# Performance work log

Measured on AMD Instinct MI355X. Metric: run time of the kernel, lower is better.

Reference implementation:

```python
import jax, jax.numpy as jnp
import numpy as np

B, S, D = 2, 2048, 1024
H = 16
DH = D // H  # 64

def setup_inputs() -> dict:
    key = jax.random.key(0)
    ks = jax.random.split(key, 7)
    sc = 1.0 / np.sqrt(DH)
    return {
        "sequences": jax.random.normal(ks[0], (B, S, D), dtype=jnp.float32),
        "Wq": jax.random.normal(ks[1], (H, DH, DH), dtype=jnp.float32) * sc,
        "bq": jax.random.normal(ks[2], (H, DH), dtype=jnp.float32) * 0.02,
        "Wk": jax.random.normal(ks[3], (H, DH, DH), dtype=jnp.float32) * sc,
        "bk": jax.random.normal(ks[4], (H, DH), dtype=jnp.float32) * 0.02,
        "Wv": jax.random.normal(ks[5], (H, DH, DH), dtype=jnp.float32) * sc,
        "bv": jax.random.normal(ks[6], (H, DH), dtype=jnp.float32) * 0.02,
    }

def reference(sequences, Wq, bq, Wk, bk, Wv, bv):
    b, s, _ = sequences.shape
    x = sequences.reshape(b, s, H, DH)  # [B,S,H,Dh]
    # torch Linear: y = x @ W^T + b; W is [out,in] => einsum contracts input dim d
    q = jnp.einsum("bshd,hed->bshe", x, Wq) + bq  # [B,S,H,Dh]
    k = jnp.einsum("bshd,hed->bshe", x, Wk) + bk
    v = jnp.einsum("bshd,hed->bshe", x, Wv) + bv
    scores = jnp.einsum("bshd,bthd->bhst", q, k) / jnp.sqrt(jnp.float32(DH))
    attn = jax.nn.softmax(scores, axis=-1)  # [B,H,S,S]
    out = jnp.einsum("bhst,bthd->bshd", attn, v)  # [B,S,H,Dh]
    return out.reshape(b, s, H * DH)
```

## Files before the change

kernel.cpp:

```cpp
#include <hip/hip_runtime.h>

typedef unsigned short u16;
typedef __bf16 bf16x8 __attribute__((ext_vector_type(8)));
typedef float  f32x4  __attribute__((ext_vector_type(4)));
typedef u16    u16x4  __attribute__((ext_vector_type(4)));

#define HH   16
#define DHH  64
#define SEQL 2048
#define NB   2
#define BHN  (NB * HH)
#define SCLF 0.1803368801111204f

static __device__ __forceinline__ u16 f2bf(float f) {
    return __builtin_bit_cast(u16, (__bf16)f);
}

static __device__ __forceinline__ void gload_lds16(const void* g, void* l) {
    __builtin_amdgcn_global_load_lds(
        (const __attribute__((address_space(1))) unsigned int*)g,
        (__attribute__((address_space(3))) unsigned int*)l, 16, 0, 0);
}

__global__ __launch_bounds__(256) void wconv_kernel(
    const float* __restrict__ Wq, const float* __restrict__ Wk,
    const float* __restrict__ Wv, u16* __restrict__ Wb)
{
    const int m = blockIdx.y;
    const float* W = (m == 0) ? Wq : (m == 1) ? Wk : Wv;
    const float s = (m == 0) ? SCLF : 1.0f;
    const int i = (blockIdx.x * 256 + threadIdx.x) * 4;
    float4 v = *reinterpret_cast<const float4*>(W + i);
    u16x4 o = { f2bf(v.x * s), f2bf(v.y * s), f2bf(v.z * s), f2bf(v.w * s) };
    *reinterpret_cast<u16x4*>(Wb + (size_t)m * 65536 + i) = o;
}

__global__ __launch_bounds__(256) void qkv_kernel(
    const float* __restrict__ x, const u16* __restrict__ Wb,
    const float* __restrict__ bq, const float* __restrict__ bk,
    const float* __restrict__ bv,
    u16* __restrict__ Qws, u16* __restrict__ Kws, u16* __restrict__ Vtws)
{
    const int h   = blockIdx.y;
    const int r0  = blockIdx.x * 64;
    const int tid = threadIdx.x;
    const int w   = tid >> 6;
    const int l   = tid & 63;
    const int c   = l & 15;
    const int g   = l >> 4;

    __shared__ u16 vt[64 * 72];

    bf16x8 xa[2];
    {
        const float* xp = x + (size_t)(r0 + w * 16 + c) * 1024 + h * 64 + g * 8;
        #pragma unroll
        for (int kh = 0; kh < 2; ++kh) {
            float4 lo = *reinterpret_cast<const float4*>(xp + kh * 32);
            float4 hi = *reinterpret_cast<const float4*>(xp + kh * 32 + 4);
            bf16x8 f;
            f[0]=(__bf16)lo.x; f[1]=(__bf16)lo.y; f[2]=(__bf16)lo.z; f[3]=(__bf16)lo.w;
            f[4]=(__bf16)hi.x; f[5]=(__bf16)hi.y; f[6]=(__bf16)hi.z; f[7]=(__bf16)hi.w;
            xa[kh] = f;
        }
    }

    const int b      = r0 >> 11;
    const int s_base = r0 & (SEQL - 1);
    const int bh     = b * HH + h;

    const float* bs[3] = {bq + h * 64, bk + h * 64, bv + h * 64};

    #pragma unroll
    for (int m = 0; m < 3; ++m) {
        const u16*   W    = Wb + (size_t)m * 65536 + h * 4096;
        const float* bias = bs[m];
        const float  bscl = (m == 0) ? SCLF : 1.0f;
        f32x4 acc[4];
        #pragma unroll
        for (int ct = 0; ct < 4; ++ct) {
            acc[ct][0] = 0.f; acc[ct][1] = 0.f; acc[ct][2] = 0.f; acc[ct][3] = 0.f;
        }
        #pragma unroll
        for (int kh = 0; kh < 2; ++kh) {
            #pragma unroll
            for (int ct = 0; ct < 4; ++ct) {
                bf16x8 wf = *reinterpret_cast<const bf16x8*>(
                    W + (ct * 16 + c) * 64 + kh * 32 + g * 8);
                acc[ct] = __builtin_amdgcn_mfma_f32_16x16x32_bf16(xa[kh], wf, acc[ct], 0, 0, 0);
            }
        }
        if (m < 2) {
            u16* outp = (m == 0 ? Qws : Kws) +
                        ((size_t)bh * SEQL + s_base + w * 16 + g * 4) * 64;
            #pragma unroll
            for (int ct = 0; ct < 4; ++ct) {
                float bb = bias[ct * 16 + c] * bscl;
                #pragma unroll
                for (int r = 0; r < 4; ++r)
                    outp[(size_t)r * 64 + ct * 16 + c] = f2bf(acc[ct][r] + bb);
            }
        } else {
            #pragma unroll
            for (int ct = 0; ct < 4; ++ct) {
                float bb = bias[ct * 16 + c];
                u16x4 pb;
                #pragma unroll
                for (int r = 0; r < 4; ++r)
                    pb[r] = f2bf(acc[ct][r] + bb);
                *reinterpret_cast<u16x4*>(&vt[(ct * 16 + c) * 72 + w * 16 + g * 4]) = pb;
            }
        }
    }
    __syncthreads();
    {
        const int d  = tid >> 2;
        const int s0 = (tid & 3) * 16;
        u16* vp = Vtws + ((size_t)bh * 64 + d) * SEQL + s_base + s0;
        uint4 v0 = *reinterpret_cast<const uint4*>(&vt[d * 72 + s0]);
        uint4 v1 = *reinterpret_cast<const uint4*>(&vt[d * 72 + s0 + 8]);
        *reinterpret_cast<uint4*>(vp)     = v0;
        *reinterpret_cast<uint4*>(vp + 8) = v1;
    }
}

__global__ __launch_bounds__(256) void attn_kernel(
    const u16* __restrict__ Qws, const u16* __restrict__ Kws,
    const u16* __restrict__ Vtws, float* __restrict__ out)
{
    const int p     = blockIdx.x;
    const int lid   = (p & 7) * 64 + (p >> 3);
    const int qtile = lid & 15;
    const int bh    = lid >> 4;
    const int b     = bh >> 4;
    const int h     = bh & 15;

    const int tid = threadIdx.x;
    const int w   = tid >> 6;
    const int l   = tid & 63;
    const int c   = l & 15;
    const int g   = l >> 4;
    const int q0  = qtile * 128 + w * 32;

    __shared__ u16 k_lds[2][64 * 64];
    __shared__ u16 v_lds[2][64 * 64];
    __shared__ u16 plds_all[4 * 32 * 64];
    char* pbase = reinterpret_cast<char*>(plds_all + w * (32 * 64));

    const u16* Kb = Kws  + (size_t)bh * SEQL * 64;
    const u16* Vb = Vtws + (size_t)bh * 64 * SEQL;

    const int rs8 = l >> 3;
    const int sx  = (l & 7) ^ rs8;

    #define STAGE(bb, k0)                                                     \
    {   _Pragma("unroll")                                                     \
        for (int a = 0; a < 2; ++a) {                                         \
            const int rbase = w * 16 + a * 8;                                 \
            const int r     = rbase + rs8;                                    \
            gload_lds16(Kb + (size_t)((k0) + r) * 64 + sx * 8,                \
                        &k_lds[bb][rbase * 64]);                              \
            gload_lds16(Vb + (size_t)r * SEQL + (k0) + sx * 8,                \
                        &v_lds[bb][rbase * 64]);                              \
        }                                                                     \
    }

    bf16x8 qf[2][2];
    #pragma unroll
    for (int qt = 0; qt < 2; ++qt)
        #pragma unroll
        for (int kh = 0; kh < 2; ++kh)
            qf[qt][kh] = *reinterpret_cast<const bf16x8*>(
                Qws + ((size_t)bh * SEQL + q0 + qt * 16 + c) * 64 + kh * 32 + g * 8);

    const f32x4 zero4 = {0.f, 0.f, 0.f, 0.f};
    bf16x8 ones8;
    #pragma unroll
    for (int j = 0; j < 8; ++j) ones8[j] = __builtin_bit_cast(__bf16, (u16)0x3F80);

    f32x4 acc[4][2];
    #pragma unroll
    for (int dt = 0; dt < 4; ++dt)
        #pragma unroll
        for (int qt = 0; qt < 2; ++qt) acc[dt][qt] = zero4;
    float mrow[2] = {-1e30f, -1e30f};
    float lrow[2] = {0.f, 0.f};

    const int rdoff = ((g ^ (c & 7)) * 8);

    bf16x8 vfA[8], vfB[8];
    bf16x8 pfA[2][2], pfB[2][2];
    f32x4  suA[2], suB[2];

    STAGE(0, 0);
    __syncthreads();

    auto body = [&](bf16x8 (&vfC)[8], bf16x8 (&pfC)[2][2], f32x4 (&suC)[2],
                    bf16x8 (&vfP)[8], bf16x8 (&pfP)[2][2], f32x4 (&suP)[2],
                    int t, bool has_prev) {
        const int cur = t & 1;

        if (t + 1 < SEQL / 64) STAGE(cur ^ 1, (t + 1) * 64);

        f32x4 st[4][2];
        __builtin_amdgcn_s_setprio(1);
        #pragma unroll
        for (int kt = 0; kt < 4; ++kt) {
            const int e0 = (kt * 16 + c) * 64 + rdoff;
            bf16x8 ka0 = *reinterpret_cast<const bf16x8*>(&k_lds[cur][e0]);
            bf16x8 ka1 = *reinterpret_cast<const bf16x8*>(&k_lds[cur][e0 ^ 32]);
            #pragma unroll
            for (int qt = 0; qt < 2; ++qt) {
                st[kt][qt] = __builtin_amdgcn_mfma_f32_16x16x32_bf16(ka0, qf[qt][0], zero4,      0, 0, 0);
                st[kt][qt] = __builtin_amdgcn_mfma_f32_16x16x32_bf16(ka1, qf[qt][1], st[kt][qt], 0, 0, 0);
            }
        }
        if (has_prev) {
            #pragma unroll
            for (int dt = 0; dt < 4; ++dt)
                #pragma unroll
                for (int qt = 0; qt < 2; ++qt) {
                    acc[dt][qt] = __builtin_amdgcn_mfma_f32_16x16x32_bf16(vfP[dt*2],   pfP[qt][0], acc[dt][qt], 0, 0, 0);
                    acc[dt][qt] = __builtin_amdgcn_mfma_f32_16x16x32_bf16(vfP[dt*2+1], pfP[qt][1], acc[dt][qt], 0, 0, 0);
                }
        }
        __builtin_amdgcn_s_setprio(0);

        #pragma unroll
        for (int dt = 0; dt < 4; ++dt) {
            const int e0 = (dt * 16 + c) * 64 + rdoff;
            vfC[dt * 2]     = *reinterpret_cast<const bf16x8*>(&v_lds[cur][e0]);
            vfC[dt * 2 + 1] = *reinterpret_cast<const bf16x8*>(&v_lds[cur][e0 ^ 32]);
        }

        #pragma unroll
        for (int qt = 0; qt < 2; ++qt) {
            if (has_prev) lrow[qt] += suP[qt][0];

            float a0 = fmaxf(st[0][qt][0], st[0][qt][1]);
            float a1 = fmaxf(st[0][qt][2], st[0][qt][3]);
            float a2 = fmaxf(st[1][qt][0], st[1][qt][1]);
            float a3 = fmaxf(st[1][qt][2], st[1][qt][3]);
            float a4 = fmaxf(st[2][qt][0], st[2][qt][1]);
            float a5 = fmaxf(st[2][qt][2], st[2][qt][3]);
            float a6 = fmaxf(st[3][qt][0], st[3][qt][1]);
            float a7 = fmaxf(st[3][qt][2], st[3][qt][3]);
            float b0 = fmaxf(fmaxf(a0, a1), fmaxf(a2, a3));
            float b1 = fmaxf(fmaxf(a4, a5), fmaxf(a6, a7));
            float mx = fmaxf(b0, b1);
            mx = fmaxf(mx, __shfl_xor(mx, 16, 64));
            mx = fmaxf(mx, __shfl_xor(mx, 32, 64));

            if (!__all(mx <= mrow[qt] + 8.f)) {
                const float mn    = fmaxf(mrow[qt], mx);
                const float alpha = __builtin_amdgcn_exp2f(mrow[qt] - mn);
                mrow[qt] = mn;
                lrow[qt] *= alpha;
                #pragma unroll
                for (int dt = 0; dt < 4; ++dt) {
                    acc[dt][qt][0] *= alpha; acc[dt][qt][1] *= alpha;
                    acc[dt][qt][2] *= alpha; acc[dt][qt][3] *= alpha;
                }
            }

            const int row = qt * 16 + c;
            #pragma unroll
            for (int kt = 0; kt < 4; ++kt) {
                u16x4 pb;
                #pragma unroll
                for (int r = 0; r < 4; ++r)
                    pb[r] = f2bf(__builtin_amdgcn_exp2f(st[kt][qt][r] - mrow[qt]));
                const int blk = (kt * 2 + (g >> 1)) ^ (row & 7);
                *reinterpret_cast<u16x4*>(pbase + row * 128 + blk * 16 + (g & 1) * 8) = pb;
            }
        }

        asm volatile("s_waitcnt lgkmcnt(0)" ::: "memory");

        #pragma unroll
        for (int qt = 0; qt < 2; ++qt) {
            const int row = qt * 16 + c;
            #pragma unroll
            for (int kh = 0; kh < 2; ++kh) {
                const int blk = (kh * 4 + g) ^ (row & 7);
                pfC[qt][kh] = *reinterpret_cast<const bf16x8*>(pbase + row * 128 + blk * 16);
            }
        }
        #pragma unroll
        for (int qt = 0; qt < 2; ++qt) {
            suC[qt] = __builtin_amdgcn_mfma_f32_16x16x32_bf16(ones8, pfC[qt][0], zero4,   0, 0, 0);
            suC[qt] = __builtin_amdgcn_mfma_f32_16x16x32_bf16(ones8, pfC[qt][1], suC[qt], 0, 0, 0);
        }

        __syncthreads();
    };

    for (int tt = 0; tt < SEQL / 64; tt += 2) {
        body(vfA, pfA, suA, vfB, pfB, suB, tt,     tt != 0);
        body(vfB, pfB, suB, vfA, pfA, suA, tt + 1, true);
    }

    #pragma unroll
    for (int dt = 0; dt < 4; ++dt)
        #pragma unroll
        for (int qt = 0; qt < 2; ++qt) {
            acc[dt][qt] = __builtin_amdgcn_mfma_f32_16x16x32_bf16(vfB[dt*2],   pfB[qt][0], acc[dt][qt], 0, 0, 0);
            acc[dt][qt] = __builtin_amdgcn_mfma_f32_16x16x32_bf16(vfB[dt*2+1], pfB[qt][1], acc[dt][qt], 0, 0, 0);
        }
    lrow[0] += suB[0][0];
    lrow[1] += suB[1][0];

    const float inv0 = 1.f / lrow[0];
    const float inv1 = 1.f / lrow[1];
    #pragma unroll
    for (int qt = 0; qt < 2; ++qt) {
        const float inv = qt ? inv1 : inv0;
        float* op = out + ((size_t)b * SEQL + q0 + qt * 16 + c) * 1024 + h * 64 + g * 4;
        #pragma unroll
        for (int dt = 0; dt < 4; ++dt) {
            float4 o;
            o.x = acc[dt][qt][0] * inv; o.y = acc[dt][qt][1] * inv;
            o.z = acc[dt][qt][2] * inv; o.w = acc[dt][qt][3] * inv;
            *reinterpret_cast<float4*>(op + dt * 16) = o;
        }
    }
}

extern "C" void kernel_launch(void* const* d_in, const int* in_sizes, int n_in,
                              void* d_out, int out_size, void* d_ws, size_t ws_size,
                              hipStream_t stream) {
    const float* x  = (const float*)d_in[0];
    const float* Wq = (const float*)d_in[1];
    const float* bq = (const float*)d_in[2];
    const float* Wk = (const float*)d_in[3];
    const float* bk = (const float*)d_in[4];
    const float* Wv = (const float*)d_in[5];
    const float* bv = (const float*)d_in[6];
    float* out = (float*)d_out;

    const size_t per = (size_t)BHN * SEQL * 64;
    u16* Qws = (u16*)d_ws;
    u16* Kws = Qws + per;
    u16* Vt  = Kws + per;
    u16* Wb  = Vt  + per;

    wconv_kernel<<<dim3(64, 3), 256, 0, stream>>>(Wq, Wk, Wv, Wb);
    qkv_kernel<<<dim3(64, 16), 256, 0, stream>>>(x, Wb, bq, bk, bv, Qws, Kws, Vt);
    attn_kernel<<<dim3(512), 256, 0, stream>>>(Qws, Kws, Vt, out);
}
```

Before: 84.98 us.

## Split attention KV range across warp pairs and merge softmax partials in LDS

Each block now handles 64 queries instead of 128. Its four waves form two pairs, and each pair processes half of the key sequence (1024 keys) with its own LDS buffer. The partial accumulators, maxima and sums are then merged through LDS at the end. This doubles the grid to 1024 blocks, which raises occupancy and parallelism across CUs. The cost is that the double-buffered prefetch goes away: each tile is now waited on with vmcnt(0) before compute, there is more K/V traffic per query, and a reduction step is added at the end.

```diff
diff --git a/kernel.cpp b/kernel.cpp
--- a/kernel.cpp
+++ b/kernel.cpp
@@ -128,24 +128,27 @@
     const u16* __restrict__ Qws, const u16* __restrict__ Kws,
     const u16* __restrict__ Vtws, float* __restrict__ out)
 {
-    const int p     = blockIdx.x;
-    const int lid   = (p & 7) * 64 + (p >> 3);
-    const int qtile = lid & 15;
-    const int bh    = lid >> 4;
-    const int b     = bh >> 4;
-    const int h     = bh & 15;
+    const int p_   = blockIdx.x;
+    const int lid  = (p_ & 7) * 128 + (p_ >> 3);
+    const int qt64 = lid & 31;
+    const int bh   = lid >> 5;
+    const int b    = bh >> 4;
+    const int h    = bh & 15;
 
     const int tid = threadIdx.x;
     const int w   = tid >> 6;
     const int l   = tid & 63;
     const int c   = l & 15;
     const int g   = l >> 4;
-    const int q0  = qtile * 128 + w * 32;
+    const int u   = w & 1;
+    const int pr  = w >> 1;
+    const int wq0 = qt64 * 64 + u * 32;
+    const int kbase = pr * 1024;
 
     __shared__ u16 k_lds[2][64 * 64];
     __shared__ u16 v_lds[2][64 * 64];
-    __shared__ u16 plds_all[4 * 32 * 64];
-    char* pbase = reinterpret_cast<char*>(plds_all + w * (32 * 64));
+    __shared__ u16 plds_all[4 * 16 * 64];
+    char* pbase = reinterpret_cast<char*>(plds_all + w * (16 * 64));
 
     const u16* Kb = Kws  + (size_t)bh * SEQL * 64;
     const u16* Vb = Vtws + (size_t)bh * 64 * SEQL;
@@ -153,25 +156,25 @@
     const int rs8 = l >> 3;
     const int sx  = (l & 7) ^ rs8;
 
-    #define STAGE(bb, k0)                                                     \
+    #define STAGE(k0)                                                         \
     {   _Pragma("unroll")                                                     \
-        for (int a = 0; a < 2; ++a) {                                         \
-            const int rbase = w * 16 + a * 8;                                 \
+        for (int a = 0; a < 4; ++a) {                                         \
+            const int rbase = u * 32 + a * 8;                                 \
             const int r     = rbase + rs8;                                    \
             gload_lds16(Kb + (size_t)((k0) + r) * 64 + sx * 8,                \
-                        &k_lds[bb][rbase * 64]);                              \
+                        &k_lds[pr][rbase * 64]);                              \
             gload_lds16(Vb + (size_t)r * SEQL + (k0) + sx * 8,                \
-                        &v_lds[bb][rbase * 64]);                              \
+                        &v_lds[pr][rbase * 64]);                              \
         }                                                                     \
     }
 
     bf16x8 qf[2][2];
     #pragma unroll
-    for (int qt = 0; qt < 2; ++qt)
+    for (int qq = 0; qq < 2; ++qq)
         #pragma unroll
         for (int kh = 0; kh < 2; ++kh)
-            qf[qt][kh] = *reinterpret_cast<const bf16x8*>(
-                Qws + ((size_t)bh * SEQL + q0 + qt * 16 + c) * 64 + kh * 32 + g * 8);
+            qf[qq][kh] = *reinterpret_cast<const bf16x8*>(
+                Qws + ((size_t)bh * SEQL + wq0 + qq * 16 + c) * 64 + kh * 32 + g * 8);
 
     const f32x4 zero4 = {0.f, 0.f, 0.f, 0.f};
     bf16x8 ones8;
@@ -182,7 +185,7 @@
     #pragma unroll
     for (int dt = 0; dt < 4; ++dt)
         #pragma unroll
-        for (int qt = 0; qt < 2; ++qt) acc[dt][qt] = zero4;
+        for (int qq = 0; qq < 2; ++qq) acc[dt][qq] = zero4;
     float mrow[2] = {-1e30f, -1e30f};
     float lrow[2] = {0.f, 0.f};
 
@@ -192,36 +195,34 @@
     bf16x8 pfA[2][2], pfB[2][2];
     f32x4  suA[2], suB[2];
 
-    STAGE(0, 0);
-    __syncthreads();
+    STAGE(kbase);
 
     auto body = [&](bf16x8 (&vfC)[8], bf16x8 (&pfC)[2][2], f32x4 (&suC)[2],
                     bf16x8 (&vfP)[8], bf16x8 (&pfP)[2][2], f32x4 (&suP)[2],
                     int t, bool has_prev) {
-        const int cur = t & 1;
-
-        if (t + 1 < SEQL / 64) STAGE(cur ^ 1, (t + 1) * 64);
+        asm volatile("s_waitcnt vmcnt(0)" ::: "memory");
+        __syncthreads();
 
         f32x4 st[4][2];
         __builtin_amdgcn_s_setprio(1);
         #pragma unroll
         for (int kt = 0; kt < 4; ++kt) {
             const int e0 = (kt * 16 + c) * 64 + rdoff;
-            bf16x8 ka0 = *reinterpret_cast<const bf16x8*>(&k_lds[cur][e0]);
-            bf16x8 ka1 = *reinterpret_cast<const bf16x8*>(&k_lds[cur][e0 ^ 32]);
-            #pragma unroll
-            for (int qt = 0; qt < 2; ++qt) {
-                st[kt][qt] = __builtin_amdgcn_mfma_f32_16x16x32_bf16(ka0, qf[qt][0], zero4,      0, 0, 0);
-                st[kt][qt] = __builtin_amdgcn_mfma_f32_16x16x32_bf16(ka1, qf[qt][1], st[kt][qt], 0, 0, 0);
+            bf16x8 ka0 = *reinterpret_cast<const bf16x8*>(&k_lds[pr][e0]);
+            bf16x8 ka1 = *reinterpret_cast<const bf16x8*>(&k_lds[pr][e0 ^ 32]);
+            #pragma unroll
+            for (int qq = 0; qq < 2; ++qq) {
+                st[kt][qq] = __builtin_amdgcn_mfma_f32_16x16x32_bf16(ka0, qf[qq][0], zero4,      0, 0, 0);
+                st[kt][qq] = __builtin_amdgcn_mfma_f32_16x16x32_bf16(ka1, qf[qq][1], st[kt][qq], 0, 0, 0);
             }
         }
         if (has_prev) {
             #pragma unroll
             for (int dt = 0; dt < 4; ++dt)
                 #pragma unroll
-                for (int qt = 0; qt < 2; ++qt) {
-                    acc[dt][qt] = __builtin_amdgcn_mfma_f32_16x16x32_bf16(vfP[dt*2],   pfP[qt][0], acc[dt][qt], 0, 0, 0);
-                    acc[dt][qt] = __builtin_amdgcn_mfma_f32_16x16x32_bf16(vfP[dt*2+1], pfP[qt][1], acc[dt][qt], 0, 0, 0);
+                for (int qq = 0; qq < 2; ++qq) {
+                    acc[dt][qq] = __builtin_amdgcn_mfma_f32_16x16x32_bf16(vfP[dt*2],   pfP[qq][0], acc[dt][qq], 0, 0, 0);
+                    acc[dt][qq] = __builtin_amdgcn_mfma_f32_16x16x32_bf16(vfP[dt*2+1], pfP[qq][1], acc[dt][qq], 0, 0, 0);
                 }
         }
         __builtin_amdgcn_s_setprio(0);
@@ -229,73 +230,71 @@
         #pragma unroll
         for (int dt = 0; dt < 4; ++dt) {
             const int e0 = (dt * 16 + c) * 64 + rdoff;
-            vfC[dt * 2]     = *reinterpret_cast<const bf16x8*>(&v_lds[cur][e0]);
-            vfC[dt * 2 + 1] = *reinterpret_cast<const bf16x8*>(&v_lds[cur][e0 ^ 32]);
-        }
-
-        #pragma unroll
-        for (int qt = 0; qt < 2; ++qt) {
-            if (has_prev) lrow[qt] += suP[qt][0];
-
-            float a0 = fmaxf(st[0][qt][0], st[0][qt][1]);
-            float a1 = fmaxf(st[0][qt][2], st[0][qt][3]);
-            float a2 = fmaxf(st[1][qt][0], st[1][qt][1]);
-            float a3 = fmaxf(st[1][qt][2], st[1][qt][3]);
-            float a4 = fmaxf(st[2][qt][0], st[2][qt][1]);
-            float a5 = fmaxf(st[2][qt][2], st[2][qt][3]);
-            float a6 = fmaxf(st[3][qt][0], st[3][qt][1]);
-            float a7 = fmaxf(st[3][qt][2], st[3][qt][3]);
+            vfC[dt * 2]     = *reinterpret_cast<const bf16x8*>(&v_lds[pr][e0]);
+            vfC[dt * 2 + 1] = *reinterpret_cast<const bf16x8*>(&v_lds[pr][e0 ^ 32]);
+        }
+
+        #pragma unroll
+        for (int qq = 0; qq < 2; ++qq) {
+            if (has_prev) lrow[qq] += suP[qq][0];
+
+            float a0 = fmaxf(st[0][qq][0], st[0][qq][1]);
+            float a1 = fmaxf(st[0][qq][2], st[0][qq][3]);
+            float a2 = fmaxf(st[1][qq][0], st[1][qq][1]);
+            float a3 = fmaxf(st[1][qq][2], st[1][qq][3]);
+            float a4 = fmaxf(st[2][qq][0], st[2][qq][1]);
+            float a5 = fmaxf(st[2][qq][2], st[2][qq][3]);
+            float a6 = fmaxf(st[3][qq][0], st[3][qq][1]);
+            float a7 = fmaxf(st[3][qq][2], st[3][qq][3]);
             float b0 = fmaxf(fmaxf(a0, a1), fmaxf(a2, a3));
             float b1 = fmaxf(fmaxf(a4, a5), fmaxf(a6, a7));
             float mx = fmaxf(b0, b1);
             mx = fmaxf(mx, __shfl_xor(mx, 16, 64));
             mx = fmaxf(mx, __shfl_xor(mx, 32, 64));
 
-            if (!__all(mx <= mrow[qt] + 8.f)) {
-                const float mn    = fmaxf(mrow[qt], mx);
-                const float alpha = __builtin_amdgcn_exp2f(mrow[qt] - mn);
-                mrow[qt] = mn;
-                lrow[qt] *= alpha;
+            if (!__all(mx <= mrow[qq] + 8.f)) {
+                const float mn    = fmaxf(mrow[qq], mx);
+                const float alpha = __builtin_amdgcn_exp2f(mrow[qq] - mn);
+                mrow[qq] = mn;
+                lrow[qq] *= alpha;
                 #pragma unroll
                 for (int dt = 0; dt < 4; ++dt) {
-                    acc[dt][qt][0] *= alpha; acc[dt][qt][1] *= alpha;
-                    acc[dt][qt][2] *= alpha; acc[dt][qt][3] *= alpha;
+                    acc[dt][qq][0] *= alpha; acc[dt][qq][1] *= alpha;
+                    acc[dt][qq][2] *= alpha; acc[dt][qq][3] *= alpha;
                 }
             }
 
-            const int row = qt * 16 + c;
             #pragma unroll
             for (int kt = 0; kt < 4; ++kt) {
                 u16x4 pb;
                 #pragma unroll
                 for (int r = 0; r < 4; ++r)
-                    pb[r] = f2bf(__builtin_amdgcn_exp2f(st[kt][qt][r] - mrow[qt]));
-                const int blk = (kt * 2 + (g >> 1)) ^ (row & 7);
-                *reinterpret_cast<u16x4*>(pbase + row * 128 + blk * 16 + (g & 1) * 8) = pb;
-            }
-        }
-
-        asm volatile("s_waitcnt lgkmcnt(0)" ::: "memory");
-
-        #pragma unroll
-        for (int qt = 0; qt < 2; ++qt) {
-            const int row = qt * 16 + c;
+                    pb[r] = f2bf(__builtin_amdgcn_exp2f(st[kt][qq][r] - mrow[qq]));
+                const int blk = (kt * 2 + (g >> 1)) ^ (c & 7);
+                *reinterpret_cast<u16x4*>(pbase + c * 128 + blk * 16 + (g & 1) * 8) = pb;
+            }
+            asm volatile("s_waitcnt lgkmcnt(0)" ::: "memory");
+            __builtin_amdgcn_sched_barrier(0);
             #pragma unroll
             for (int kh = 0; kh < 2; ++kh) {
-                const int blk = (kh * 4 + g) ^ (row & 7);
-                pfC[qt][kh] = *reinterpret_cast<const bf16x8*>(pbase + row * 128 + blk * 16);
-            }
-        }
-        #pragma unroll
-        for (int qt = 0; qt < 2; ++qt) {
-            suC[qt] = __builtin_amdgcn_mfma_f32_16x16x32_bf16(ones8, pfC[qt][0], zero4,   0, 0, 0);
-            suC[qt] = __builtin_amdgcn_mfma_f32_16x16x32_bf16(ones8, pfC[qt][1], suC[qt], 0, 0, 0);
+                const int blk = (kh * 4 + g) ^ (c & 7);
+                pfC[qq][kh] = *reinterpret_cast<const bf16x8*>(pbase + c * 128 + blk * 16);
+            }
+            asm volatile("s_waitcnt lgkmcnt(0)" ::: "memory");
+            __builtin_amdgcn_sched_barrier(0);
+        }
+
+        #pragma unroll
+        for (int qq = 0; qq < 2; ++qq) {
+            suC[qq] = __builtin_amdgcn_mfma_f32_16x16x32_bf16(ones8, pfC[qq][0], zero4,   0, 0, 0);
+            suC[qq] = __builtin_amdgcn_mfma_f32_16x16x32_bf16(ones8, pfC[qq][1], suC[qq], 0, 0, 0);
         }
 
         __syncthreads();
+        if (t + 1 < 16) STAGE(kbase + (t + 1) * 64);
     };
 
-    for (int tt = 0; tt < SEQL / 64; tt += 2) {
+    for (int tt = 0; tt < 16; tt += 2) {
         body(vfA, pfA, suA, vfB, pfB, suB, tt,     tt != 0);
         body(vfB, pfB, suB, vfA, pfA, suA, tt + 1, true);
     }
@@ -303,25 +302,50 @@
     #pragma unroll
     for (int dt = 0; dt < 4; ++dt)
         #pragma unroll
-        for (int qt = 0; qt < 2; ++qt) {
-            acc[dt][qt] = __builtin_amdgcn_mfma_f32_16x16x32_bf16(vfB[dt*2],   pfB[qt][0], acc[dt][qt], 0, 0, 0);
-            acc[dt][qt] = __builtin_amdgcn_mfma_f32_16x16x32_bf16(vfB[dt*2+1], pfB[qt][1], acc[dt][qt], 0, 0, 0);
+        for (int qq = 0; qq < 2; ++qq) {
+            acc[dt][qq] = __builtin_amdgcn_mfma_f32_16x16x32_bf16(vfB[dt*2],   pfB[qq][0], acc[dt][qq], 0, 0, 0);
+            acc[dt][qq] = __builtin_amdgcn_mfma_f32_16x16x32_bf16(vfB[dt*2+1], pfB[qq][1], acc[dt][qq], 0, 0, 0);
         }
     lrow[0] += suB[0][0];
     lrow[1] += suB[1][0];
 
-    const float inv0 = 1.f / lrow[0];
-    const float inv1 = 1.f / lrow[1];
-    #pragma unroll
-    for (int qt = 0; qt < 2; ++qt) {
-        const float inv = qt ? inv1 : inv0;
-        float* op = out + ((size_t)b * SEQL + q0 + qt * 16 + c) * 1024 + h * 64 + g * 4;
-        #pragma unroll
-        for (int dt = 0; dt < 4; ++dt) {
-            float4 o;
-            o.x = acc[dt][qt][0] * inv; o.y = acc[dt][qt][1] * inv;
-            o.z = acc[dt][qt][2] * inv; o.w = acc[dt][qt][3] * inv;
-            *reinterpret_cast<float4*>(op + dt * 16) = o;
+    if (w >= 2) {
+        float* s = ((w == 2) ? (float*)k_lds : (float*)v_lds) + l * 36;
+        #pragma unroll
+        for (int dt = 0; dt < 4; ++dt)
+            #pragma unroll
+            for (int qq = 0; qq < 2; ++qq)
+                #pragma unroll
+                for (int r = 0; r < 4; ++r)
+                    s[dt * 8 + qq * 4 + r] = acc[dt][qq][r];
+        s[32] = mrow[0]; s[33] = mrow[1]; s[34] = lrow[0]; s[35] = lrow[1];
+    }
+    __syncthreads();
+    if (w < 2) {
+        const float* s = ((w == 0) ? (const float*)k_lds : (const float*)v_lds) + l * 36;
+        const float mB[2] = {s[32], s[33]};
+        const float lB[2] = {s[34], s[35]};
+        float inv[2];
+        float aA[2], aB[2];
+        #pragma unroll
+        for (int qq = 0; qq < 2; ++qq) {
+            const float mn = fmaxf(mrow[qq], mB[qq]);
+            aA[qq] = __builtin_amdgcn_exp2f(mrow[qq] - mn);
+            aB[qq] = __builtin_amdgcn_exp2f(mB[qq]  - mn);
+            inv[qq] = 1.f / (lrow[qq] * aA[qq] + lB[qq] * aB[qq]);
+        }
+        #pragma unroll
+        for (int qq = 0; qq < 2; ++qq) {
+            float* op = out + ((size_t)b * SEQL + wq0 + qq * 16 + c) * 1024 + h * 64 + g * 4;
+            #pragma unroll
+            for (int dt = 0; dt < 4; ++dt) {
+                float4 o;
+                #pragma unroll
+                for (int r = 0; r < 4; ++r)
+                    ((float*)&o)[r] = (acc[dt][qq][r] * aA[qq] +
+                                       s[dt * 8 + qq * 4 + r] * aB[qq]) * inv[qq];
+                *reinterpret_cast<float4*>(op + dt * 16) = o;
+            }
         }
     }
 }
@@ -346,5 +370,5 @@
 
     wconv_kernel<<<dim3(64, 3), 256, 0, stream>>>(Wq, Wk, Wv, Wb);
     qkv_kernel<<<dim3(64, 16), 256, 0, stream>>>(x, Wb, bq, bk, bv, Qws, Kws, Vt);
-    attn_kernel<<<dim3(512), 256, 0, stream>>>(Qws, Kws, Vt, out);
-}
+    attn_kernel<<<dim3(1024), 256, 0, stream>>>(Qws, Kws, Vt, out);
+}
```

Result: slower. 96.10 us (+13.1%).
